# Optimization experiments

Measured on AMD Instinct MI355X. Metric: run time of the kernel, lower is better.

The kernel has to match this reference:

```python
import jax, jax.numpy as jnp
import numpy as np

B, NW = 1024, 300
N = NW // 3          # 100 tokens (keypoints)
E = 5                # token dim after cat of PE(2): 3 + 2
H, D, L = 4, 64, 3   # heads, d_attention, layers


def setup_inputs() -> dict:
    key = jax.random.key(0)
    ks = jax.random.split(key, 8)
    s = jnp.float32(0.1)
    x = jax.random.normal(ks[0], (B, NW), dtype=jnp.float32)
    Wq = jax.random.normal(ks[1], (L, H, D, E), dtype=jnp.float32) * s  # per-head W_Q (no bias)
    Wk = jax.random.normal(ks[2], (L, H, D, E), dtype=jnp.float32) * s
    Wv = jax.random.normal(ks[3], (L, H, D, E), dtype=jnp.float32) * s
    Wo = jax.random.normal(ks[4], (L, E, H * D), dtype=jnp.float32) * s  # MHA output proj (no bias)
    Wf = jax.random.normal(ks[5], (L, E, E), dtype=jnp.float32) * s      # FFN linear
    bf = jax.random.normal(ks[6], (L, E), dtype=jnp.float32) * s
    g1 = jnp.ones((L, E), dtype=jnp.float32)
    b1 = jnp.zeros((L, E), dtype=jnp.float32)
    g2 = jnp.ones((L, E), dtype=jnp.float32)
    b2 = jnp.zeros((L, E), dtype=jnp.float32)
    return dict(x=x, Wq=Wq, Wk=Wk, Wv=Wv, Wo=Wo, Wf=Wf, bf=bf,
                g1=g1, b1=b1, g2=g2, b2=b2)


def _layer_norm(x, g, b, eps=1e-5):
    mu = jnp.mean(x, axis=-1, keepdims=True)
    var = jnp.mean((x - mu) ** 2, axis=-1, keepdims=True)  # biased, like torch LN
    return (x - mu) / jnp.sqrt(var + eps) * g + b


def reference(x, Wq, Wk, Wv, Wo, Wf, bf, g1, b1, g2, b2):
    kp = x.reshape(B, N, 3)                      # 'b (n d) -> b n d', d=3
    mask = kp[:, :, -1] > 0                      # [B,N] keypoint confidence mask
    # PositionalEncoding(d_model=2, kind='cat'): div_term=[1] -> pe=[sin(pos),cos(pos)]
    pos = jnp.arange(N, dtype=jnp.float32)
    pe = jnp.stack([jnp.sin(pos), jnp.cos(pos)], axis=-1)         # [N,2]
    out = jnp.concatenate([kp, jnp.broadcast_to(pe, (B, N, 2))], axis=-1)  # [B,N,5]
    out = jnp.where(mask[:, :, None], out, jnp.float32(0.0))      # out[~mask]=0

    pair = mask[:, None, None, :] & mask[:, None, :, None]        # [B,1,N,N]
    neg = -jnp.finfo(jnp.float32).max
    scale = jnp.float32(1.0 / np.sqrt(D))
    for l in range(L):
        # per-head projections (heads vectorized over h)
        q = jnp.einsum('bne,hde->bhnd', out, Wq[l])
        k = jnp.einsum('bne,hde->bhnd', out, Wk[l])
        v = jnp.einsum('bne,hde->bhnd', out, Wv[l])
        dots = jnp.einsum('bhid,bhjd->bhij', q, k) * scale        # [B,H,N,N]
        dots = jnp.where(pair, dots, neg)
        attn = jax.nn.softmax(dots, axis=-1)
        o = jnp.einsum('bhij,bhjd->bhid', attn, v)                # [B,H,N,D]
        o = o.transpose(0, 2, 1, 3).reshape(B, N, H * D)          # concat heads
        attn_out = o @ Wo[l].T                                    # [B,N,E]
        ln1 = _layer_norm(attn_out + out, g1[l], b1[l])
        ffn = jax.nn.relu(ln1 @ Wf[l].T + bf[l])
        out = _layer_norm(ffn + ln1, g2[l], b2[l])
    return out
```

## Files before the change

### kernel.cpp

```cpp
#include <hip/hip_runtime.h>
#include <math.h>

#define NTOK 100
#define EDIM 5
#define NH   4
#define NL   3
#define DD   64
#define BLK  128

__device__ __forceinline__ float fexp2(float x){ float r; asm("v_exp_f32 %0, %1" : "=v"(r) : "v"(x)); return r; }
__device__ __forceinline__ float frcp (float x){ float r; asm("v_rcp_f32 %0, %1" : "=v"(r) : "v"(x)); return r; }
__device__ __forceinline__ float frsq (float x){ float r; asm("v_rsq_f32 %0, %1" : "=v"(r) : "v"(x)); return r; }
#define RL(v, l) __int_as_float(__builtin_amdgcn_readlane(__float_as_int(v), (l)))

__global__ void precompute_mp(const float* __restrict__ Wq,
                              const float* __restrict__ Wk,
                              const float* __restrict__ Wv,
                              const float* __restrict__ Wo,
                              float* __restrict__ mp) {
  const int blk = blockIdx.x;
  const int which = blk / 12;
  const int rem = blk % 12;
  const int l = rem / 4, h = rem % 4;
  const int t = threadIdx.x;

  __shared__ float A[320];
  __shared__ float Bsh[320];

  const float* wa = (which ? Wv : Wq) + (l*NH + h)*DD*EDIM;
  for (int r = t; r < 320; r += 64) A[r] = wa[r];
  if (which == 0) {
    const float* wk = Wk + (l*NH + h)*DD*EDIM;
    for (int r = t; r < 320; r += 64) Bsh[r] = wk[r];
  } else {
    for (int r = t; r < 320; r += 64) {
      int f = r >> 6, d = r & 63;
      Bsh[r] = Wo[(l*EDIM + f)*(NH*DD) + h*DD + d];
    }
  }
  __syncthreads();
  if (t < 25) {
    int e = t / 5, f = t % 5;
    float acc = 0.f;
    if (which == 0) {
      #pragma unroll 8
      for (int d = 0; d < DD; ++d) acc += A[d*5+e] * Bsh[d*5+f];
      acc *= 0.125f * 1.44269504088896340736f;
    } else {
      #pragma unroll 8
      for (int d = 0; d < DD; ++d) acc += A[d*5+e] * Bsh[f*64+d];
    }
    mp[which*960 + ((l*NH + h)*EDIM + e)*8 + f] = acc;
  }
}

__global__ __launch_bounds__(BLK, 2) void encoder_kernel(
    const float* __restrict__ x,
    const float* __restrict__ mp,
    const float* __restrict__ Wf,
    const float* __restrict__ bfv,
    const float* __restrict__ g1,
    const float* __restrict__ b1,
    const float* __restrict__ g2,
    const float* __restrict__ b2,
    float* __restrict__ out)
{
  const int b = blockIdx.x, t = threadIdx.x;
  const int wv = t >> 6, ln = t & 63;

  __shared__ float4 s_MP4[480];
  __shared__ float4 s_wp4[2][2][104];
  __shared__ float  s_wp1[2][2][104];
  __shared__ float4 s_i4[104];
  __shared__ float  s_i1[104];
  __shared__ float  s_cf[152];
  __shared__ int    s_cidx[NTOK];
  __shared__ unsigned long long s_bal[2];

  const float* mpf = (const float*)s_MP4;
  for (int r = t; r < 480; r += BLK) s_MP4[r] = ((const float4*)mp)[r];
  for (int r = t; r < 104; r += BLK) { s_i4[r] = make_float4(0.f,0.f,0.f,0.f); s_i1[r] = 0.f; }
  for (int r = t; r < 150; r += BLK) {
    float v;
    if      (r <  75) v = Wf[r];
    else if (r <  90) v = bfv[r-75];
    else if (r < 105) v = g1[r-90];
    else if (r < 120) v = b1[r-105];
    else if (r < 135) v = g2[r-120];
    else              v = b2[r-135];
    s_cf[r] = v;
  }

  float k0=0.f, k1=0.f, k2=0.f, msk=0.f;
  if (t < NTOK) {
    k0 = x[b*300 + 3*t];
    k1 = x[b*300 + 3*t + 1];
    k2 = x[b*300 + 3*t + 2];
    msk = (k2 > 0.f) ? 1.f : 0.f;
  }
  unsigned long long bal = __ballot(t < NTOK && msk != 0.f);
  if (t == 0)  s_bal[0] = bal;
  if (t == 64) s_bal[1] = bal;
  __syncthreads();
  const unsigned long long bw0 = s_bal[0], bw1 = s_bal[1];
  const int nm = __builtin_amdgcn_readfirstlane(__popcll(bw0) + __popcll(bw1));
  if (t < NTOK) {
    int lane = t & 63;
    unsigned long long lm = (lane == 0) ? 0ull : ((1ull << lane) - 1ull);
    int pre = (t < 64) ? __popcll(bw0 & lm) : (__popcll(bw0) + __popcll(bw1 & lm));
    if (msk != 0.f) {
      s_i4[pre] = make_float4(k0, k1, k2, __sinf((float)t));
      s_i1[pre] = __cosf((float)t);
      s_cidx[t] = pre;
    } else {
      s_cidx[t] = nm;
    }
  }
  __syncthreads();

  const int rows = nm + 1;
  const bool twoRows = (rows > 64);
  const int jhiA = (nm < 64) ? nm : 64;
  const float wext = (float)(NTOK - nm);

  float oA0,oA1,oA2,oA3,oA4, oB0,oB1,oB2,oB3,oB4;
  { float4 v = s_i4[ln]; oA0=v.x; oA1=v.y; oA2=v.z; oA3=v.w; oA4=s_i1[ln]; }
  if (twoRows && ln < 40) {
    float4 v = s_i4[ln+64]; oB0=v.x; oB1=v.y; oB2=v.z; oB3=v.w; oB4=s_i1[ln+64];
  } else { oB0=0.f; oB1=0.f; oB2=0.f; oB3=0.f; oB4=0.f; }

  int bufp = 0;
  float cSA[5], cSB[5];

  for (int l = 0; l < NL; ++l) {
    const float* M0 = mpf + ((l*NH + 2*wv    )*EDIM)*8;
    const float* M1 = mpf + ((l*NH + 2*wv + 1)*EDIM)*8;
    const float* P0 = mpf + 960 + ((l*NH + 2*wv    )*EDIM)*8;
    const float* P1 = mpf + 960 + ((l*NH + 2*wv + 1)*EDIM)*8;

    auto attn_row = [&](float o0,float o1,float o2,float o3,float o4,
                        int row, float (&cS)[5]) {
      float oc[5] = {o0,o1,o2,o3,o4};
      float a00=0.f,a01=0.f,a02=0.f,a03=0.f,a04=0.f;
      float a10=0.f,a11=0.f,a12=0.f,a13=0.f,a14=0.f;
      #pragma unroll
      for (int e = 0; e < 5; ++e) {
        float4 m0 = *(const float4*)(M0 + e*8); float m04 = M0[e*8+4];
        float4 m1 = *(const float4*)(M1 + e*8); float m14 = M1[e*8+4];
        float v = oc[e];
        a00 += v*m0.x; a01 += v*m0.y; a02 += v*m0.z; a03 += v*m0.w; a04 += v*m04;
        a10 += v*m1.x; a11 += v*m1.y; a12 += v*m1.z; a13 += v*m1.w; a14 += v*m14;
      }
      const bool rep = (row == nm);
      if (rep) {
        a00=0.f;a01=0.f;a02=0.f;a03=0.f;a04=0.f;
        a10=0.f;a11=0.f;a12=0.f;a13=0.f;a14=0.f;
      }
      float ls0=0.f, ls1=0.f;
      float w00=0.f,w01=0.f,w02=0.f,w03=0.f,w04=0.f;
      float w10=0.f,w11=0.f,w12=0.f,w13=0.f,w14=0.f;
      #pragma unroll 4
      for (int j = 0; j < jhiA; ++j) {
        float ox = RL(oA0,j), oy = RL(oA1,j), oz = RL(oA2,j),
              ow = RL(oA3,j), oe = RL(oA4,j);
        float s0 = (a00*ox + a01*oy) + ((a02*oz + a03*ow) + a04*oe);
        float s1 = (a10*ox + a11*oy) + ((a12*oz + a13*ow) + a14*oe);
        float p0 = fexp2(s0), p1 = fexp2(s1);
        ls0 += p0; ls1 += p1;
        w00 += p0*ox; w01 += p0*oy; w02 += p0*oz; w03 += p0*ow; w04 += p0*oe;
        w10 += p1*ox; w11 += p1*oy; w12 += p1*oz; w13 += p1*ow; w14 += p1*oe;
      }
      if (twoRows) {
        #pragma unroll 4
        for (int j = 64; j < nm; ++j) {
          int jl = j - 64;
          float ox = RL(oB0,jl), oy = RL(oB1,jl), oz = RL(oB2,jl),
                ow = RL(oB3,jl), oe = RL(oB4,jl);
          float s0 = (a00*ox + a01*oy) + ((a02*oz + a03*ow) + a04*oe);
          float s1 = (a10*ox + a11*oy) + ((a12*oz + a13*ow) + a14*oe);
          float p0 = fexp2(s0), p1 = fexp2(s1);
          ls0 += p0; ls1 += p1;
          w00 += p0*ox; w01 += p0*oy; w02 += p0*oz; w03 += p0*ow; w04 += p0*oe;
          w10 += p1*ox; w11 += p1*oy; w12 += p1*oz; w13 += p1*ow; w14 += p1*oe;
        }
      }
      if (rep) {
        w00 += wext*o0; w01 += wext*o1; w02 += wext*o2; w03 += wext*o3; w04 += wext*o4;
        w10 += wext*o0; w11 += wext*o1; w12 += wext*o2; w13 += wext*o3; w14 += wext*o4;
      }
      float inv0 = rep ? 0.01f : frcp(ls0);
      float inv1 = rep ? 0.01f : frcp(ls1);
      float wc0[5] = {w00*inv0, w01*inv0, w02*inv0, w03*inv0, w04*inv0};
      float wc1[5] = {w10*inv1, w11*inv1, w12*inv1, w13*inv1, w14*inv1};
      float c0=0.f,c1=0.f,c2=0.f,c3=0.f,c4=0.f;
      #pragma unroll
      for (int e = 0; e < 5; ++e) {
        float4 pr = *(const float4*)(P0 + e*8); float p4 = P0[e*8+4];
        c0 += wc0[e]*pr.x; c1 += wc0[e]*pr.y; c2 += wc0[e]*pr.z;
        c3 += wc0[e]*pr.w; c4 += wc0[e]*p4;
      }
      #pragma unroll
      for (int e = 0; e < 5; ++e) {
        float4 pr = *(const float4*)(P1 + e*8); float p4 = P1[e*8+4];
        c0 += wc1[e]*pr.x; c1 += wc1[e]*pr.y; c2 += wc1[e]*pr.z;
        c3 += wc1[e]*pr.w; c4 += wc1[e]*p4;
      }
      cS[0]=c0; cS[1]=c1; cS[2]=c2; cS[3]=c3; cS[4]=c4;
      s_wp4[bufp][wv][row] = make_float4(c0,c1,c2,c3);
      s_wp1[bufp][wv][row] = c4;
    };

    attn_row(oA0,oA1,oA2,oA3,oA4, ln, cSA);
    if (twoRows && ln < 40) attn_row(oB0,oB1,oB2,oB3,oB4, ln+64, cSB);
    __syncthreads();

    auto upd = [&](float& p0,float& p1,float& p2,float& p3,float& p4,
                   float (&cS)[5], int row) {
      if (row >= rows) return;
      float4 wo = s_wp4[bufp][wv^1][row];
      float wo4 = s_wp1[bufp][wv^1][row];
      float y0 = p0 + cS[0] + wo.x,  y1 = p1 + cS[1] + wo.y;
      float y2 = p2 + cS[2] + wo.z,  y3 = p3 + cS[3] + wo.w;
      float y4 = p4 + cS[4] + wo4;
      float yv[5] = {y0,y1,y2,y3,y4};
      float mu = 0.2f*(y0+y1+y2+y3+y4);
      float var = 0.f;
      #pragma unroll
      for (int e = 0; e < 5; ++e) { float d = yv[e]-mu; var += d*d; }
      float iv = frsq(var*0.2f + 1e-5f);
      float l1[5];
      #pragma unroll
      for (int e = 0; e < 5; ++e)
        l1[e] = (yv[e]-mu)*iv*s_cf[90+l*5+e] + s_cf[105+l*5+e];
      float r2[5];
      #pragma unroll
      for (int e = 0; e < 5; ++e) {
        float acc = s_cf[75+l*5+e];
        #pragma unroll
        for (int f = 0; f < 5; ++f) acc += l1[f]*s_cf[l*25+e*5+f];
        acc = acc > 0.f ? acc : 0.f;
        r2[e] = acc + l1[e];
      }
      float mu2 = 0.2f*(r2[0]+r2[1]+r2[2]+r2[3]+r2[4]);
      float var2 = 0.f;
      #pragma unroll
      for (int e = 0; e < 5; ++e) { float d = r2[e]-mu2; var2 += d*d; }
      float iv2 = frsq(var2*0.2f + 1e-5f);
      p0 = (r2[0]-mu2)*iv2*s_cf[120+l*5+0] + s_cf[135+l*5+0];
      p1 = (r2[1]-mu2)*iv2*s_cf[120+l*5+1] + s_cf[135+l*5+1];
      p2 = (r2[2]-mu2)*iv2*s_cf[120+l*5+2] + s_cf[135+l*5+2];
      p3 = (r2[3]-mu2)*iv2*s_cf[120+l*5+3] + s_cf[135+l*5+3];
      p4 = (r2[4]-mu2)*iv2*s_cf[120+l*5+4] + s_cf[135+l*5+4];
    };
    upd(oA0,oA1,oA2,oA3,oA4, cSA, ln);
    if (twoRows && ln < 40) upd(oB0,oB1,oB2,oB3,oB4, cSB, ln+64);
    bufp ^= 1;
  }

  if (wv == 0) {
    if (ln < rows) { s_i4[ln] = make_float4(oA0,oA1,oA2,oA3); s_i1[ln] = oA4; }
    if (twoRows && (ln + 64 < rows)) {
      s_i4[ln+64] = make_float4(oB0,oB1,oB2,oB3); s_i1[ln+64] = oB4;
    }
  }
  __syncthreads();
  for (int r = t; r < NTOK*EDIM; r += BLK) {
    int i = r / EDIM;
    int e = r - i*EDIM;
    int c = s_cidx[i];
    float v = (e < 4) ? ((const float*)&s_i4[c])[e] : s_i1[c];
    out[b*(NTOK*EDIM) + r] = v;
  }
}

extern "C" void kernel_launch(void* const* d_in, const int* in_sizes, int n_in,
                              void* d_out, int out_size, void* d_ws, size_t ws_size,
                              hipStream_t stream) {
  const float* x  = (const float*)d_in[0];
  const float* Wq = (const float*)d_in[1];
  const float* Wk = (const float*)d_in[2];
  const float* Wv = (const float*)d_in[3];
  const float* Wo = (const float*)d_in[4];
  const float* Wf = (const float*)d_in[5];
  const float* bf = (const float*)d_in[6];
  const float* g1 = (const float*)d_in[7];
  const float* b1 = (const float*)d_in[8];
  const float* g2 = (const float*)d_in[9];
  const float* b2 = (const float*)d_in[10];
  float* outp = (float*)d_out;
  float* mp   = (float*)d_ws;

  precompute_mp<<<24, 64, 0, stream>>>(Wq, Wk, Wv, Wo, mp);
  encoder_kernel<<<1024, BLK, 0, stream>>>(x, mp, Wf, bf, g1, b1, g2, b2, outp);
}
```

Before: 131.0 us.

## Use one wavefront per batch computing all four heads, dropping cross-wave exchange

Each block shrinks from two wavefronts (two heads each) to a single 64-lane wavefront that processes all four heads per row. The shared-memory exchange of per-wave partial attention outputs and the per-layer __syncthreads go away, and the mask ballot is built directly inside the one wave. The cost is more register pressure from holding four heads' accumulators, less parallelism per batch element, and launch bounds relaxed to allow one wave per block.

After: 138.9 us. 6.0% more time.

```diff
diff --git a/kernel.cpp b/kernel.cpp
--- a/kernel.cpp
+++ b/kernel.cpp
@@ -6,7 +6,7 @@
 #define NH   4
 #define NL   3
 #define DD   64
-#define BLK  128
+#define BLK  64
 
 __device__ __forceinline__ float fexp2(float x){ float r; asm("v_exp_f32 %0, %1" : "=v"(r) : "v"(x)); return r; }
 __device__ __forceinline__ float frcp (float x){ float r; asm("v_rcp_f32 %0, %1" : "=v"(r) : "v"(x)); return r; }
@@ -54,7 +54,7 @@
   }
 }
 
-__global__ __launch_bounds__(BLK, 2) void encoder_kernel(
+__global__ __launch_bounds__(BLK, 1) void encoder_kernel(
     const float* __restrict__ x,
     const float* __restrict__ mp,
     const float* __restrict__ Wf,
@@ -65,22 +65,18 @@
     const float* __restrict__ b2,
     float* __restrict__ out)
 {
-  const int b = blockIdx.x, t = threadIdx.x;
-  const int wv = t >> 6, ln = t & 63;
+  const int b = blockIdx.x, ln = threadIdx.x;
 
   __shared__ float4 s_MP4[480];
-  __shared__ float4 s_wp4[2][2][104];
-  __shared__ float  s_wp1[2][2][104];
   __shared__ float4 s_i4[104];
   __shared__ float  s_i1[104];
   __shared__ float  s_cf[152];
   __shared__ int    s_cidx[NTOK];
-  __shared__ unsigned long long s_bal[2];
 
   const float* mpf = (const float*)s_MP4;
-  for (int r = t; r < 480; r += BLK) s_MP4[r] = ((const float4*)mp)[r];
-  for (int r = t; r < 104; r += BLK) { s_i4[r] = make_float4(0.f,0.f,0.f,0.f); s_i1[r] = 0.f; }
-  for (int r = t; r < 150; r += BLK) {
+  for (int r = ln; r < 480; r += 64) s_MP4[r] = ((const float4*)mp)[r];
+  for (int r = ln; r < 104; r += 64) { s_i4[r] = make_float4(0.f,0.f,0.f,0.f); s_i1[r] = 0.f; }
+  for (int r = ln; r < 150; r += 64) {
     float v;
     if      (r <  75) v = Wf[r];
     else if (r <  90) v = bfv[r-75];
@@ -90,31 +86,32 @@
     else              v = b2[r-135];
     s_cf[r] = v;
   }
-
-  float k0=0.f, k1=0.f, k2=0.f, msk=0.f;
-  if (t < NTOK) {
-    k0 = x[b*300 + 3*t];
-    k1 = x[b*300 + 3*t + 1];
-    k2 = x[b*300 + 3*t + 2];
-    msk = (k2 > 0.f) ? 1.f : 0.f;
-  }
-  unsigned long long bal = __ballot(t < NTOK && msk != 0.f);
-  if (t == 0)  s_bal[0] = bal;
-  if (t == 64) s_bal[1] = bal;
-  __syncthreads();
-  const unsigned long long bw0 = s_bal[0], bw1 = s_bal[1];
-  const int nm = __builtin_amdgcn_readfirstlane(__popcll(bw0) + __popcll(bw1));
-  if (t < NTOK) {
-    int lane = t & 63;
-    unsigned long long lm = (lane == 0) ? 0ull : ((1ull << lane) - 1ull);
-    int pre = (t < 64) ? __popcll(bw0 & lm) : (__popcll(bw0) + __popcll(bw1 & lm));
-    if (msk != 0.f) {
-      s_i4[pre] = make_float4(k0, k1, k2, __sinf((float)t));
-      s_i1[pre] = __cosf((float)t);
-      s_cidx[t] = pre;
-    } else {
-      s_cidx[t] = nm;
-    }
+  __syncthreads();
+
+  float kA0 = x[b*300 + 3*ln], kA1 = x[b*300 + 3*ln + 1], kA2 = x[b*300 + 3*ln + 2];
+  bool mA = (kA2 > 0.f);
+  float kB0 = 0.f, kB1 = 0.f, kB2 = 0.f; bool mB = false;
+  if (ln < 36) {
+    kB0 = x[b*300 + 192 + 3*ln]; kB1 = x[b*300 + 193 + 3*ln]; kB2 = x[b*300 + 194 + 3*ln];
+    mB = (kB2 > 0.f);
+  }
+  unsigned long long bal0 = __ballot(mA);
+  unsigned long long bal1 = __ballot(ln < 36 && mB);
+  const int nm = __builtin_amdgcn_readfirstlane(__popcll(bal0) + __popcll(bal1));
+  unsigned long long lm = (ln == 0) ? 0ull : ((1ull << ln) - 1ull);
+  int preA = __popcll(bal0 & lm);
+  int preB = __popcll(bal0) + __popcll(bal1 & lm);
+  if (mA) {
+    s_i4[preA] = make_float4(kA0, kA1, kA2, __sinf((float)ln));
+    s_i1[preA] = __cosf((float)ln);
+    s_cidx[ln] = preA;
+  } else s_cidx[ln] = nm;
+  if (ln < 36) {
+    if (mB) {
+      s_i4[preB] = make_float4(kB0, kB1, kB2, __sinf((float)(ln+64)));
+      s_i1[preB] = __cosf((float)(ln+64));
+      s_cidx[ln+64] = preB;
+    } else s_cidx[ln+64] = nm;
   }
   __syncthreads();
 
@@ -129,99 +126,93 @@
     float4 v = s_i4[ln+64]; oB0=v.x; oB1=v.y; oB2=v.z; oB3=v.w; oB4=s_i1[ln+64];
   } else { oB0=0.f; oB1=0.f; oB2=0.f; oB3=0.f; oB4=0.f; }
 
-  int bufp = 0;
-  float cSA[5], cSB[5];
-
   for (int l = 0; l < NL; ++l) {
-    const float* M0 = mpf + ((l*NH + 2*wv    )*EDIM)*8;
-    const float* M1 = mpf + ((l*NH + 2*wv + 1)*EDIM)*8;
-    const float* P0 = mpf + 960 + ((l*NH + 2*wv    )*EDIM)*8;
-    const float* P1 = mpf + 960 + ((l*NH + 2*wv + 1)*EDIM)*8;
+    const float* Mb = mpf + (l*NH*EDIM)*8;
+    const float* Pb = mpf + 960 + (l*NH*EDIM)*8;
 
     auto attn_row = [&](float o0,float o1,float o2,float o3,float o4,
                         int row, float (&cS)[5]) {
       float oc[5] = {o0,o1,o2,o3,o4};
-      float a00=0.f,a01=0.f,a02=0.f,a03=0.f,a04=0.f;
-      float a10=0.f,a11=0.f,a12=0.f,a13=0.f,a14=0.f;
-      #pragma unroll
-      for (int e = 0; e < 5; ++e) {
-        float4 m0 = *(const float4*)(M0 + e*8); float m04 = M0[e*8+4];
-        float4 m1 = *(const float4*)(M1 + e*8); float m14 = M1[e*8+4];
-        float v = oc[e];
-        a00 += v*m0.x; a01 += v*m0.y; a02 += v*m0.z; a03 += v*m0.w; a04 += v*m04;
-        a10 += v*m1.x; a11 += v*m1.y; a12 += v*m1.z; a13 += v*m1.w; a14 += v*m14;
+      float A[NH][5];
+      #pragma unroll
+      for (int h = 0; h < NH; ++h) {
+        #pragma unroll
+        for (int f = 0; f < 5; ++f) A[h][f] = 0.f;
+        #pragma unroll
+        for (int e = 0; e < 5; ++e) {
+          const float* Mr = Mb + (h*5+e)*8;
+          float4 m4 = *(const float4*)Mr; float m1 = Mr[4];
+          float v = oc[e];
+          A[h][0] += v*m4.x; A[h][1] += v*m4.y; A[h][2] += v*m4.z;
+          A[h][3] += v*m4.w; A[h][4] += v*m1;
+        }
       }
       const bool rep = (row == nm);
       if (rep) {
-        a00=0.f;a01=0.f;a02=0.f;a03=0.f;a04=0.f;
-        a10=0.f;a11=0.f;a12=0.f;a13=0.f;a14=0.f;
-      }
-      float ls0=0.f, ls1=0.f;
-      float w00=0.f,w01=0.f,w02=0.f,w03=0.f,w04=0.f;
-      float w10=0.f,w11=0.f,w12=0.f,w13=0.f,w14=0.f;
-      #pragma unroll 4
+        #pragma unroll
+        for (int h = 0; h < NH; ++h)
+          { A[h][0]=0.f; A[h][1]=0.f; A[h][2]=0.f; A[h][3]=0.f; A[h][4]=0.f; }
+      }
+      float W[NH][5], LS[NH];
+      #pragma unroll
+      for (int h = 0; h < NH; ++h) {
+        LS[h]=0.f; W[h][0]=0.f; W[h][1]=0.f; W[h][2]=0.f; W[h][3]=0.f; W[h][4]=0.f;
+      }
+      #pragma unroll 2
       for (int j = 0; j < jhiA; ++j) {
         float ox = RL(oA0,j), oy = RL(oA1,j), oz = RL(oA2,j),
               ow = RL(oA3,j), oe = RL(oA4,j);
-        float s0 = (a00*ox + a01*oy) + ((a02*oz + a03*ow) + a04*oe);
-        float s1 = (a10*ox + a11*oy) + ((a12*oz + a13*ow) + a14*oe);
-        float p0 = fexp2(s0), p1 = fexp2(s1);
-        ls0 += p0; ls1 += p1;
-        w00 += p0*ox; w01 += p0*oy; w02 += p0*oz; w03 += p0*ow; w04 += p0*oe;
-        w10 += p1*ox; w11 += p1*oy; w12 += p1*oz; w13 += p1*ow; w14 += p1*oe;
+        #pragma unroll
+        for (int h = 0; h < NH; ++h) {
+          float s = (A[h][0]*ox + A[h][1]*oy) + ((A[h][2]*oz + A[h][3]*ow) + A[h][4]*oe);
+          float p = fexp2(s);
+          LS[h] += p;
+          W[h][0] += p*ox; W[h][1] += p*oy; W[h][2] += p*oz;
+          W[h][3] += p*ow; W[h][4] += p*oe;
+        }
       }
       if (twoRows) {
-        #pragma unroll 4
+        #pragma unroll 2
         for (int j = 64; j < nm; ++j) {
           int jl = j - 64;
           float ox = RL(oB0,jl), oy = RL(oB1,jl), oz = RL(oB2,jl),
                 ow = RL(oB3,jl), oe = RL(oB4,jl);
-          float s0 = (a00*ox + a01*oy) + ((a02*oz + a03*ow) + a04*oe);
-          float s1 = (a10*ox + a11*oy) + ((a12*oz + a13*ow) + a14*oe);
-          float p0 = fexp2(s0), p1 = fexp2(s1);
-          ls0 += p0; ls1 += p1;
-          w00 += p0*ox; w01 += p0*oy; w02 += p0*oz; w03 += p0*ow; w04 += p0*oe;
-          w10 += p1*ox; w11 += p1*oy; w12 += p1*oz; w13 += p1*ow; w14 += p1*oe;
+          #pragma unroll
+          for (int h = 0; h < NH; ++h) {
+            float s = (A[h][0]*ox + A[h][1]*oy) + ((A[h][2]*oz + A[h][3]*ow) + A[h][4]*oe);
+            float p = fexp2(s);
+            LS[h] += p;
+            W[h][0] += p*ox; W[h][1] += p*oy; W[h][2] += p*oz;
+            W[h][3] += p*ow; W[h][4] += p*oe;
+          }
         }
       }
       if (rep) {
-        w00 += wext*o0; w01 += wext*o1; w02 += wext*o2; w03 += wext*o3; w04 += wext*o4;
-        w10 += wext*o0; w11 += wext*o1; w12 += wext*o2; w13 += wext*o3; w14 += wext*o4;
-      }
-      float inv0 = rep ? 0.01f : frcp(ls0);
-      float inv1 = rep ? 0.01f : frcp(ls1);
-      float wc0[5] = {w00*inv0, w01*inv0, w02*inv0, w03*inv0, w04*inv0};
-      float wc1[5] = {w10*inv1, w11*inv1, w12*inv1, w13*inv1, w14*inv1};
-      float c0=0.f,c1=0.f,c2=0.f,c3=0.f,c4=0.f;
-      #pragma unroll
-      for (int e = 0; e < 5; ++e) {
-        float4 pr = *(const float4*)(P0 + e*8); float p4 = P0[e*8+4];
-        c0 += wc0[e]*pr.x; c1 += wc0[e]*pr.y; c2 += wc0[e]*pr.z;
-        c3 += wc0[e]*pr.w; c4 += wc0[e]*p4;
-      }
-      #pragma unroll
-      for (int e = 0; e < 5; ++e) {
-        float4 pr = *(const float4*)(P1 + e*8); float p4 = P1[e*8+4];
-        c0 += wc1[e]*pr.x; c1 += wc1[e]*pr.y; c2 += wc1[e]*pr.z;
-        c3 += wc1[e]*pr.w; c4 += wc1[e]*p4;
-      }
-      cS[0]=c0; cS[1]=c1; cS[2]=c2; cS[3]=c3; cS[4]=c4;
-      s_wp4[bufp][wv][row] = make_float4(c0,c1,c2,c3);
-      s_wp1[bufp][wv][row] = c4;
+        #pragma unroll
+        for (int h = 0; h < NH; ++h) {
+          W[h][0] += wext*o0; W[h][1] += wext*o1; W[h][2] += wext*o2;
+          W[h][3] += wext*o3; W[h][4] += wext*o4;
+        }
+      }
+      cS[0]=0.f; cS[1]=0.f; cS[2]=0.f; cS[3]=0.f; cS[4]=0.f;
+      #pragma unroll
+      for (int h = 0; h < NH; ++h) {
+        float inv = rep ? 0.01f : frcp(LS[h]);
+        #pragma unroll
+        for (int e = 0; e < 5; ++e) {
+          const float* Pr = Pb + (h*5+e)*8;
+          float4 p4 = *(const float4*)Pr; float p1 = Pr[4];
+          float we = W[h][e] * inv;
+          cS[0] += we*p4.x; cS[1] += we*p4.y; cS[2] += we*p4.z;
+          cS[3] += we*p4.w; cS[4] += we*p1;
+        }
+      }
     };
 
-    attn_row(oA0,oA1,oA2,oA3,oA4, ln, cSA);
-    if (twoRows && ln < 40) attn_row(oB0,oB1,oB2,oB3,oB4, ln+64, cSB);
-    __syncthreads();
-
     auto upd = [&](float& p0,float& p1,float& p2,float& p3,float& p4,
-                   float (&cS)[5], int row) {
-      if (row >= rows) return;
-      float4 wo = s_wp4[bufp][wv^1][row];
-      float wo4 = s_wp1[bufp][wv^1][row];
-      float y0 = p0 + cS[0] + wo.x,  y1 = p1 + cS[1] + wo.y;
-      float y2 = p2 + cS[2] + wo.z,  y3 = p3 + cS[3] + wo.w;
-      float y4 = p4 + cS[4] + wo4;
+                   const float (&cS)[5]) {
+      float y0 = p0 + cS[0], y1 = p1 + cS[1], y2 = p2 + cS[2];
+      float y3 = p3 + cS[3], y4 = p4 + cS[4];
       float yv[5] = {y0,y1,y2,y3,y4};
       float mu = 0.2f*(y0+y1+y2+y3+y4);
       float var = 0.f;
@@ -252,19 +243,20 @@
       p3 = (r2[3]-mu2)*iv2*s_cf[120+l*5+3] + s_cf[135+l*5+3];
       p4 = (r2[4]-mu2)*iv2*s_cf[120+l*5+4] + s_cf[135+l*5+4];
     };
-    upd(oA0,oA1,oA2,oA3,oA4, cSA, ln);
-    if (twoRows && ln < 40) upd(oB0,oB1,oB2,oB3,oB4, cSB, ln+64);
-    bufp ^= 1;
-  }
-
-  if (wv == 0) {
-    if (ln < rows) { s_i4[ln] = make_float4(oA0,oA1,oA2,oA3); s_i1[ln] = oA4; }
-    if (twoRows && (ln + 64 < rows)) {
-      s_i4[ln+64] = make_float4(oB0,oB1,oB2,oB3); s_i1[ln+64] = oB4;
-    }
-  }
-  __syncthreads();
-  for (int r = t; r < NTOK*EDIM; r += BLK) {
+
+    float cSA[5], cSB[5];
+    attn_row(oA0,oA1,oA2,oA3,oA4, ln, cSA);
+    if (twoRows) attn_row(oB0,oB1,oB2,oB3,oB4, ln+64, cSB);
+    upd(oA0,oA1,oA2,oA3,oA4, cSA);
+    if (twoRows) upd(oB0,oB1,oB2,oB3,oB4, cSB);
+  }
+
+  if (ln < rows) { s_i4[ln] = make_float4(oA0,oA1,oA2,oA3); s_i1[ln] = oA4; }
+  if (twoRows && (ln + 64 < rows)) {
+    s_i4[ln+64] = make_float4(oB0,oB1,oB2,oB3); s_i1[ln+64] = oB4;
+  }
+  __syncthreads();
+  for (int r = ln; r < NTOK*EDIM; r += 64) {
     int i = r / EDIM;
     int e = r - i*EDIM;
     int c = s_cidx[i];
```
